# Optimization experiments

Hardware: AMD Instinct MI355X
Metric: run time of the kernel (lower is better)

## Reference

```python
import jax, jax.numpy as jnp
import numpy as np

K = 20
EPS = 1e-5
SLOPE = 0.2


def setup_inputs() -> dict:
    key = jax.random.key(0)
    k1, k2 = jax.random.split(key, 2)
    B, C, N, O = 2, 64, 8192, 64
    x = jax.random.normal(k1, (B, C, N), dtype=jnp.float32)
    W = jax.random.normal(k2, (O, 2 * C), dtype=jnp.float32) * 0.05  # Conv2d 1x1, bias=False
    gamma = jnp.ones((O,), dtype=jnp.float32)
    beta = jnp.zeros((O,), dtype=jnp.float32)
    return {"x": x, "W": W, "gamma": gamma, "beta": beta}


def reference(x, W, gamma, beta):
    # x: (B, C, N)
    B, C, N = x.shape
    xt = jnp.swapaxes(x, 1, 2)  # (B, N, C)

    # --- get_GraphFeatures: KNN by negative squared euclidean distance ---
    inner = jnp.einsum('bnc,bmc->bnm', xt, xt)          # (B, N, N)
    sq = jnp.sum(xt * xt, axis=-1)                      # (B, N)
    neg_dist = 2.0 * inner - sq[:, :, None] - sq[:, None, :]
    _, idx = jax.lax.top_k(neg_dist, K)                 # (B, N, K) int32

    # gather neighbor features: (B, N, K, C)
    nbr = jax.vmap(lambda pts, i: pts[i])(xt, idx)
    center = xt[:, :, None, :]                          # (B, N, 1, C)
    # edge feature: concat(x_j - x_i, x_i) -> (B, N, K, 2C)
    edge = jnp.concatenate([nbr - center, jnp.broadcast_to(center, nbr.shape)], axis=-1)

    # --- 1x1 conv (pointwise GEMM) -> (B, O, N, K) ---
    h = jnp.einsum('bnkf,of->bonk', edge, W)

    # --- BatchNorm2d (training-mode batch stats over B, N, K per channel) ---
    mean = jnp.mean(h, axis=(0, 2, 3), keepdims=True)
    var = jnp.var(h, axis=(0, 2, 3), keepdims=True)
    h = (h - mean) * jax.lax.rsqrt(var + EPS)
    h = h * gamma[None, :, None, None] + beta[None, :, None, None]

    # --- LeakyReLU(0.2) + max over neighbors ---
    h = jnp.where(h >= 0, h, SLOPE * h)
    return jnp.max(h, axis=-1)                          # (B, O, N)
```

## Files before the change

### kernel.cpp

```cpp
#include <hip/hip_runtime.h>
#include <cfloat>

#define BB 2
#define NN 8192
#define OO 64
#define KK 20
#define QB 128
#define MS 16
#define CHUNK 512
#define CAPQ 192
#define RB 8
#define RBS 9

using f16x8  = __attribute__((ext_vector_type(8))) _Float16;
using f32x16 = __attribute__((ext_vector_type(16))) float;
typedef unsigned long long u64;

#define XH_OFF ((size_t)0)
#define XL_OFF (XH_OFF + (size_t)BB*NN*32)
#define SQ_OFF (XL_OFF + (size_t)BB*NN*32)
#define Y1_OFF (SQ_OFF + (size_t)BB*NN)
#define Y2_OFF (Y1_OFF + (size_t)BB*NN*64)
#define TH_OFF (Y2_OFF + (size_t)BB*NN*64)
#define CN_OFF (TH_OFF + (size_t)BB*NN)
#define TL_OFF (CN_OFF + (size_t)BB*NN)
#define CA_OFF (TL_OFF + (size_t)2*BB*NN*KK)
#define IX_OFF (CA_OFF + (size_t)BB*NN*CAPQ*2)
#define HX_OFF (IX_OFF + (size_t)BB*NN*KK)
#define HN_OFF (HX_OFF + (size_t)BB*NN*64)
#define ST_OFF (HN_OFF + (size_t)BB*NN*64)

__device__ __forceinline__ size_t frag_off(int b, int tile, int t, int lane) {
    return ((((size_t)b * (NN / 32) + tile) * 4 + t) * 64 + lane) * 8;
}

__device__ __forceinline__ unsigned fmap(float f) {
    unsigned u = __float_as_uint(f);
    return (u & 0x80000000u) ? ~u : (u | 0x80000000u);
}

__device__ __forceinline__ void sort16(float* v) {
#pragma unroll
    for (int k = 2; k <= 16; k <<= 1) {
#pragma unroll
        for (int j = k >> 1; j > 0; j >>= 1) {
#pragma unroll
            for (int i = 0; i < 16; ++i) {
                int l = i ^ j;
                if (l > i) {
                    bool up = ((i & k) == 0);
                    float mn = fminf(v[i], v[l]);
                    float mx = fmaxf(v[i], v[l]);
                    v[i] = up ? mn : mx;
                    v[l] = up ? mx : mn;
                }
            }
        }
    }
}
__device__ __forceinline__ void bmerge32(float* A) {
#pragma unroll
    for (int j = 16; j > 0; j >>= 1) {
#pragma unroll
        for (int i = 0; i < 32; ++i) {
            if ((i & j) == 0) {
                float mn = fminf(A[i], A[i | j]);
                float mx = fmaxf(A[i], A[i | j]);
                A[i] = mn;
                A[i | j] = mx;
            }
        }
    }
}
__device__ __forceinline__ void merge32_16(float* A, const float* B) {
#pragma unroll
    for (int i = 16; i < 32; ++i) A[i] = fminf(A[i], B[31 - i]);
    bmerge32(A);
}
__device__ __forceinline__ void merge32_32(float* A, const float* B) {
    float t[32];
#pragma unroll
    for (int i = 0; i < 32; ++i) t[i] = fminf(A[i], B[31 - i]);
    bmerge32(t);
#pragma unroll
    for (int i = 0; i < 32; ++i) A[i] = t[i];
}

__device__ __forceinline__ void load_atile(const _Float16* __restrict__ xh,
                                           const _Float16* __restrict__ xl,
                                           int b, int ptile, int lane,
                                           f16x8* Ah, f16x8* Al) {
#pragma unroll
    for (int t = 0; t < 4; ++t) {
        size_t o = frag_off(b, ptile, t, lane);
        Ah[t] = *(const f16x8*)&xh[o];
        Al[t] = *(const f16x8*)&xl[o];
    }
}

__device__ __forceinline__ void dist_from_frags(const f16x8* Ah, const f16x8* Al,
                                                const float* sqs, int sbase, int kh,
                                                const f16x8* Qh, const f16x8* Ql,
                                                float* dv) {
    f32x16 c0, c1;
#pragma unroll
    for (int r2 = 0; r2 < 4; ++r2) {
        float4 sv = *(const float4*)&sqs[sbase + 8 * r2 + 4 * kh];
        c0[4 * r2 + 0] = sv.x;
        c0[4 * r2 + 1] = sv.y;
        c0[4 * r2 + 2] = sv.z;
        c0[4 * r2 + 3] = sv.w;
    }
#pragma unroll
    for (int i = 0; i < 16; ++i) c1[i] = 0.f;
#pragma unroll
    for (int t = 0; t < 4; ++t) {
        c0 = __builtin_amdgcn_mfma_f32_32x32x16_f16(Ah[t], Qh[t], c0, 0, 0, 0);
        c1 = __builtin_amdgcn_mfma_f32_32x32x16_f16(Ah[t], Ql[t], c1, 0, 0, 0);
        c1 = __builtin_amdgcn_mfma_f32_32x32x16_f16(Al[t], Qh[t], c1, 0, 0, 0);
    }
#pragma unroll
    for (int i = 0; i < 16; ++i)
        dv[i] = fmaf(-2.f, c0[i], -9.765625e-4f * c1[i]);
}

__device__ __forceinline__ void load_qfrag(const _Float16* __restrict__ xh,
                                           const _Float16* __restrict__ xl,
                                           int b, int qbase, int lane,
                                           f16x8* Qh, f16x8* Ql) {
    const int qtile = qbase >> 5;
#pragma unroll
    for (int t = 0; t < 4; ++t) {
        size_t o = frag_off(b, qtile, t, lane);
        Qh[t] = *(const f16x8*)&xh[o];
        Ql[t] = *(const f16x8*)&xl[o];
    }
}

__global__ void __launch_bounds__(256, 2)
kA(const float* __restrict__ x, const float* __restrict__ W,
   float* __restrict__ ws) {
    __shared__ __align__(16) float w1s[32 * 64];
    __shared__ __align__(16) float w2s[32 * 64];
    __shared__ float xs[64 * 65];
    __shared__ float tb[64 * 33];
    const int bb = blockIdx.z;
    const int og = blockIdx.y;
    const int obase = og * 32;
    const int nbase = blockIdx.x * 64;
    const int tn = threadIdx.x & 63, tq = threadIdx.x >> 6;

    for (int i = threadIdx.x; i < 2048; i += 256) {
        int ol = i >> 6, c = i & 63;
        float a = W[(obase + ol) * 128 + c];
        float d = W[(obase + ol) * 128 + 64 + c];
        w1s[i] = a;
        w2s[i] = d - a;
    }
    for (int i = threadIdx.x; i < 4096; i += 256) {
        int c = i >> 6, nl = i & 63;
        xs[c * 65 + nl] = x[((size_t)bb * 64 + c) * NN + nbase + nl];
    }
    if (og == 0) {
        if (blockIdx.x == 0 && bb == 0 && threadIdx.x < 128)
            ws[ST_OFF + threadIdx.x] = 0.f;
        int gid = (bb * 128 + blockIdx.x) * 256 + threadIdx.x;
        if (gid < BB * NN) ((int*)(ws + CN_OFF))[gid] = 0;
    }
    __syncthreads();

    float xc[64];
#pragma unroll
    for (int c = 0; c < 64; ++c) xc[c] = xs[c * 65 + tn];

    if (og == 0 && tq == 0) {
        float sqv = 0.f;
#pragma unroll
        for (int c = 0; c < 64; ++c) sqv = fmaf(xc[c], xc[c], sqv);
        int n = nbase + tn;
        ws[SQ_OFF + (size_t)bb * NN + n] = sqv;
        _Float16* xh = (_Float16*)(ws + XH_OFF);
        _Float16* xl = (_Float16*)(ws + XL_OFF);
        int tile = n >> 5, r = n & 31;
#pragma unroll
        for (int t = 0; t < 4; ++t) {
#pragma unroll
            for (int kh = 0; kh < 2; ++kh) {
                f16x8 vh, vl;
#pragma unroll
                for (int j = 0; j < 8; ++j) {
                    float v = xc[t * 16 + kh * 8 + j];
                    _Float16 h = (_Float16)v;
                    vh[j] = h;
                    vl[j] = (_Float16)((v - (float)h) * 2048.f);
                }
                size_t o = frag_off(bb, tile, t, kh * 32 + r);
                *(f16x8*)&xh[o] = vh;
                *(f16x8*)&xl[o] = vl;
            }
        }
    }

    float a1v[8], a2v[8];
#pragma unroll
    for (int o2 = 0; o2 < 8; ++o2) {
        int ol = tq * 8 + o2;
        const float4* w1v = (const float4*)&w1s[ol * 64];
        const float4* w2v = (const float4*)&w2s[ol * 64];
        float a1 = 0.f, a2 = 0.f;
#pragma unroll
        for (int c4 = 0; c4 < 16; ++c4) {
            float4 v1 = w1v[c4];
            float4 v2 = w2v[c4];
            a1 = fmaf(v1.x, xc[4*c4],   a1);
            a1 = fmaf(v1.y, xc[4*c4+1], a1);
            a1 = fmaf(v1.z, xc[4*c4+2], a1);
            a1 = fmaf(v1.w, xc[4*c4+3], a1);
            a2 = fmaf(v2.x, xc[4*c4],   a2);
            a2 = fmaf(v2.y, xc[4*c4+1], a2);
            a2 = fmaf(v2.z, xc[4*c4+2], a2);
            a2 = fmaf(v2.w, xc[4*c4+3], a2);
        }
        a1v[o2] = a1;
        a2v[o2] = a2;
    }

    const int lo = threadIdx.x & 31;
    const int lp = (threadIdx.x >> 5) & 1;
#pragma unroll
    for (int o2 = 0; o2 < 8; ++o2)
        tb[tn * 33 + tq * 8 + o2] = a1v[o2];
    __syncthreads();
#pragma unroll
    for (int j = 0; j < 8; ++j) {
        int r = tq * 16 + 2 * j + lp;
        ws[Y1_OFF + ((size_t)bb * NN + nbase + r) * 64 + obase + lo] = tb[r * 33 + lo];
    }
    __syncthreads();
#pragma unroll
    for (int o2 = 0; o2 < 8; ++o2)
        tb[tn * 33 + tq * 8 + o2] = a2v[o2];
    __syncthreads();
#pragma unroll
    for (int j = 0; j < 8; ++j) {
        int r = tq * 16 + 2 * j + lp;
        ws[Y2_OFF + ((size_t)bb * NN + nbase + r) * 64 + obase + lo] = tb[r * 33 + lo];
    }
}

__global__ void __launch_bounds__(256, 3)
kT(const _Float16* __restrict__ xh, const _Float16* __restrict__ xl,
   const float* __restrict__ sq, float* __restrict__ thrL) {
    __shared__ float mrg[32 * 128];
    __shared__ __align__(16) float sqs[1024];
    const int tid  = threadIdx.x;
    const int lane = tid & 63;
    const int wv   = tid >> 6;
    const int qcol = lane & 31;
    const int kh   = lane >> 5;
    const int b     = blockIdx.y >> 1;
    const int s     = blockIdx.y & 1;
    const int qbase = blockIdx.x * 32;

    for (int i = tid; i < 1024; i += 256)
        sqs[i] = -0.5f * sq[(size_t)b * NN + s * 1024 + i];

    f16x8 Qh[4], Ql[4];
    load_qfrag(xh, xl, b, qbase, lane, Qh, Ql);
    __syncthreads();

    float dk[32];
#pragma unroll
    for (int i = 0; i < 32; ++i) dk[i] = FLT_MAX;

    const int p0 = s * 1024 + wv * 256;
    for (int pt = p0; pt < p0 + 256; pt += 32) {
        f16x8 Ah[4], Al[4];
        load_atile(xh, xl, b, pt >> 5, lane, Ah, Al);
        float dv[16];
        dist_from_frags(Ah, Al, sqs, pt - s * 1024, kh, Qh, Ql, dv);
        float m16 = dv[0];
#pragma unroll
        for (int i = 1; i < 16; ++i) m16 = fminf(m16, dv[i]);
        if (__any(m16 < dk[KK - 1])) {
            sort16(dv);
            merge32_16(dk, dv);
        }
    }

    {
        float B[32];
#pragma unroll
        for (int j = 0; j < 32; ++j) B[j] = __shfl(dk[j], lane | 32);
        merge32_32(dk, B);
    }
    if (kh == 0) {
#pragma unroll
        for (int j = 0; j < 32; ++j) mrg[j * 128 + wv * 32 + qcol] = dk[j];
    }
    __syncthreads();

    if (tid < 32) {
        float B[32];
#pragma unroll 1
        for (int w = 1; w < 4; ++w) {
#pragma unroll
            for (int j = 0; j < 32; ++j) B[j] = mrg[j * 128 + w * 32 + tid];
            merge32_32(dk, B);
        }
        size_t base = (((size_t)b * 2 + s) * NN + qbase + tid) * KK;
#pragma unroll
        for (int j = 0; j < KK; ++j) thrL[base + j] = dk[j];
    }
}

__global__ void kM2(const float* __restrict__ thrL, float* __restrict__ thr) {
    int gid = blockIdx.x * 256 + threadIdx.x;
    int b = gid >> 13, q = gid & (NN - 1);
    float A[KK], Bv[KK];
    const float4* pa = (const float4*)&thrL[(((size_t)b * 2 + 0) * NN + q) * KK];
    const float4* pb = (const float4*)&thrL[(((size_t)b * 2 + 1) * NN + q) * KK];
#pragma unroll
    for (int i = 0; i < 5; ++i) {
        float4 va = pa[i];
        float4 vb = pb[i];
        A[4*i] = va.x;  A[4*i+1] = va.y;  A[4*i+2] = va.z;  A[4*i+3] = va.w;
        Bv[4*i] = vb.x; Bv[4*i+1] = vb.y; Bv[4*i+2] = vb.z; Bv[4*i+3] = vb.w;
    }
    float v = fminf(Bv[KK - 1], A[KK - 1]);
#pragma unroll
    for (int i = 1; i < KK; ++i)
        v = fminf(v, fmaxf(A[i - 1], Bv[KK - 1 - i]));
    thr[gid] = v + fabsf(v) * 1e-6f + 1e-6f;
}

__global__ void __launch_bounds__(256, 4)
kS(const _Float16* __restrict__ xh, const _Float16* __restrict__ xl,
   const float* __restrict__ sq, const float* __restrict__ thr,
   int* __restrict__ cnt, u64* __restrict__ cand) {
    __shared__ u64 lbuf[256 * RBS];
    __shared__ __align__(16) float sqs[CHUNK];
    const int tid  = threadIdx.x;
    const int lane = tid & 63;
    const int wv   = tid >> 6;
    const int qcol = lane & 31;
    const int kh   = lane >> 5;
    const int id     = blockIdx.x;
    const int ychunk = id & 15;
    const int qt     = (id >> 4) & 63;
    const int b      = (id >> 10) & 1;
    const int qbase  = qt * QB + wv * 32;
    const int pbase0 = ychunk * CHUNK;
    const int ptile0 = pbase0 >> 5;

    for (int i = tid; i < CHUNK; i += 256)
        sqs[i] = -0.5f * sq[(size_t)b * NN + pbase0 + i];

    f16x8 Qh[4], Ql[4];
    load_qfrag(xh, xl, b, qbase, lane, Qh, Ql);

    const size_t qidx = (size_t)b * NN + qbase + qcol;
    const float tv = thr[qidx];
    const size_t cb = qidx * CAPQ;
    int c_ = 0;

    __syncthreads();

    auto flushS = [&]() {
        if (c_ > 0) {
            int base = atomicAdd(&cnt[qidx], c_);
#pragma unroll 1
            for (int j = 0; j < c_; ++j) {
                int slot = base + j;
                if (slot < CAPQ) cand[cb + slot] = lbuf[tid * RBS + j];
            }
            c_ = 0;
        }
    };

#pragma unroll 2
    for (int tt = 0; tt < CHUNK / 32; ++tt) {
        f16x8 Ah[4], Al[4];
        load_atile(xh, xl, b, ptile0 + tt, lane, Ah, Al);
        float dv[16];
        dist_from_frags(Ah, Al, sqs, tt * 32, kh, Qh, Ql, dv);

        const int pb4 = pbase0 + tt * 32 + 4 * kh;
#pragma unroll
        for (int i = 0; i < 16; ++i) {
            float d = dv[i];
            if (d <= tv) {
                int id2 = pb4 + ((i & 3) + 8 * (i >> 2));
                lbuf[tid * RBS + c_] = ((u64)fmap(d) << 32) | (unsigned)id2;
                if (++c_ == RB) flushS();
            }
        }
    }
    flushS();
}

__global__ void __launch_bounds__(64)
kP(const int* __restrict__ cnt, const u64* __restrict__ cand,
   int* __restrict__ idxK) {
    const int lane = threadIdx.x;
    const int qloc = lane & 31;
    const int par  = lane >> 5;
    const int q = blockIdx.x * 32 + qloc;
    int m = cnt[q];
    m = m < CAPQ ? m : CAPQ;
    const int nj = (m - par + 1) >> 1;
    u64 kk[KK];
#pragma unroll
    for (int i = 0; i < KK; ++i) kk[i] = ~0ull;

    auto insU = [&](u64 v) {
        kk[KK - 1] = v;
#pragma unroll
        for (int i = KK - 1; i > 0; --i) {
            u64 a = kk[i - 1], c = kk[i];
            bool sw = c < a;
            kk[i - 1] = sw ? c : a;
            kk[i]     = sw ? a : c;
        }
    };

    const u64* cp = &cand[(size_t)q * CAPQ + par];
#pragma unroll 1
    for (int j = 0; j < CAPQ / 2; ++j) {
        if (!__any(j < nj)) break;
        u64 v = cp[2 * j];
        if ((j < nj) && v < kk[KK - 1]) insU(v);
    }

#pragma unroll
    for (int j = 0; j < KK; ++j) {
        u64 v = __shfl(kk[j], lane | 32);
        bool ins = (par == 0) && v < kk[KK - 1];
        if (!__any(ins)) break;
        if (ins) insU(v);
    }

    if (par == 0) {
        int* op = &idxK[(size_t)q * KK];
#pragma unroll
        for (int i = 0; i < KK; ++i) op[i] = (int)(unsigned)(kk[i] & 0xffffffffu);
    }
}

__global__ void kC1(const float* __restrict__ y1, const float* __restrict__ y2,
                    const int* __restrict__ idxK, float* __restrict__ hmaxT,
                    float* __restrict__ hminT, float* __restrict__ stats) {
    __shared__ int li[32 * KK];
    __shared__ float red[256];
    __shared__ float thm[32 * 65];
    __shared__ float thn[32 * 65];
    int b = blockIdx.y;
    int o = threadIdx.x & 63;
    int nn = threadIdx.x >> 6;
    int nbase = blockIdx.x * 32;

    for (int i = threadIdx.x; i < 32 * KK; i += 256)
        li[i] = idxK[((size_t)b * NN + nbase) * KK + i];
    __syncthreads();

    float s = 0.f, ss = 0.f;
    for (int gidx = 0; gidx < 8; ++gidx) {
        int nl = gidx * 4 + nn;
        int n = nbase + nl;
        float y2v = y2[((size_t)b * NN + n) * 64 + o];
        float hm = -FLT_MAX, hn = FLT_MAX;
        const int* lin = &li[nl * KK];
#pragma unroll 4
        for (int k = 0; k < KK; ++k) {
            int j = lin[k];
            float h = y1[((size_t)b * NN + j) * 64 + o] + y2v;
            s += h;
            ss += h * h;
            hm = fmaxf(hm, h);
            hn = fminf(hn, h);
        }
        thm[nl * 65 + o] = hm;
        thn[nl * 65 + o] = hn;
    }
    __syncthreads();

    int l = threadIdx.x & 31, g = threadIdx.x >> 5;
#pragma unroll
    for (int i = 0; i < 8; ++i) {
        int o2 = g * 8 + i;
        hmaxT[((size_t)b * 64 + o2) * NN + nbase + l] = thm[l * 65 + o2];
        hminT[((size_t)b * 64 + o2) * NN + nbase + l] = thn[l * 65 + o2];
    }

    __syncthreads();
    red[threadIdx.x] = s;
    __syncthreads();
    if (threadIdx.x < 64) {
        float v = red[o] + red[64 + o] + red[128 + o] + red[192 + o];
        atomicAdd(&stats[o], v);
    }
    __syncthreads();
    red[threadIdx.x] = ss;
    __syncthreads();
    if (threadIdx.x < 64) {
        float v = red[o] + red[64 + o] + red[128 + o] + red[192 + o];
        atomicAdd(&stats[64 + o], v);
    }
}

__global__ void kC3(const float* __restrict__ hmaxT, const float* __restrict__ hminT,
                    const float* __restrict__ stats, const float* __restrict__ gamma,
                    const float* __restrict__ beta, float* __restrict__ out) {
    int o = blockIdx.x;
    int half = blockIdx.y;
    int b = blockIdx.z;
    const float c = (float)BB * NN * KK;
    float mean = stats[o] / c;
    float var = stats[64 + o] / c - mean * mean;
    float rs = rsqrtf(var + 1e-5f);
    float a = gamma[o] * rs;
    float b2 = beta[o] - a * mean;
    size_t rowb = ((size_t)b * 64 + o) * NN;
    int n0 = half * (NN / 2), n1 = n0 + NN / 2;
    for (int n = n0 + threadIdx.x; n < n1; n += 256) {
        float hm = hmaxT[rowb + n];
        float hn = hminT[rowb + n];
        float hs = (a >= 0.f) ? hm : hn;
        float v = a * hs + b2;
        v = (v >= 0.f) ? v : 0.2f * v;
        out[rowb + n] = v;
    }
}

extern "C" void kernel_launch(void* const* d_in, const int* in_sizes, int n_in,
                              void* d_out, int out_size, void* d_ws, size_t ws_size,
                              hipStream_t stream) {
    const float* x     = (const float*)d_in[0];
    const float* W     = (const float*)d_in[1];
    const float* gamma = (const float*)d_in[2];
    const float* beta  = (const float*)d_in[3];
    float* out = (float*)d_out;
    float* ws  = (float*)d_ws;

    _Float16* xh = (_Float16*)(ws + XH_OFF);
    _Float16* xl = (_Float16*)(ws + XL_OFF);
    float* sq    = ws + SQ_OFF;
    float* y1    = ws + Y1_OFF;
    float* y2    = ws + Y2_OFF;
    float* thr   = ws + TH_OFF;
    int*   cnt   = (int*)(ws + CN_OFF);
    float* thrL  = ws + TL_OFF;
    u64*   cand  = (u64*)(ws + CA_OFF);
    int*   idxK  = (int*)(ws + IX_OFF);
    float* hmaxT = ws + HX_OFF;
    float* hminT = ws + HN_OFF;
    float* stats = ws + ST_OFF;

    kA<<<dim3(NN / 64, 2, BB), 256, 0, stream>>>(x, W, ws);
    kT<<<dim3(NN / 32, 2 * BB), 256, 0, stream>>>(xh, xl, sq, thrL);
    kM2<<<dim3(BB * NN / 256), 256, 0, stream>>>(thrL, thr);
    kS<<<dim3(MS * (NN / QB) * BB), 256, 0, stream>>>(xh, xl, sq, thr, cnt, cand);
    kP<<<dim3(BB * NN / 32), 64, 0, stream>>>(cnt, cand, idxK);
    kC1<<<dim3(NN / 32, BB), 256, 0, stream>>>(y1, y2, idxK, hmaxT, hminT, stats);
    kC3<<<dim3(OO, 2, BB), 256, 0, stream>>>(hmaxT, hminT, stats, gamma, beta, out);
}
```

Before: 261.2 us.

## Replace per-thread insertion top-k with wave-wide rank counting selection

The candidate selection kernel used to assign each query to two threads, each running a serial 20-element insertion sort over up to 192 candidates, then merged them through shuffles. Now a whole 64-lane wave handles one query: each lane holds up to three candidates, computes each one's rank by broadcasting every candidate with shuffles and counting smaller keys, and scatters the candidates with rank below K directly to the output. This removes the long serial compare-swap chains and the divergent inserts in exchange for O(m) shuffles per lane and 8x more waves. It relies on the packed distance/index keys being unique so the ranks do not collide.

```diff
diff --git a/kernel.cpp b/kernel.cpp
--- a/kernel.cpp
+++ b/kernel.cpp
@@ -399,52 +399,50 @@
     flushS();
 }
 
-__global__ void __launch_bounds__(64)
+__global__ void __launch_bounds__(256, 4)
 kP(const int* __restrict__ cnt, const u64* __restrict__ cand,
    int* __restrict__ idxK) {
-    const int lane = threadIdx.x;
-    const int qloc = lane & 31;
-    const int par  = lane >> 5;
-    const int q = blockIdx.x * 32 + qloc;
+    const int lane = threadIdx.x & 63;
+    const int wq   = threadIdx.x >> 6;
+    const int q    = blockIdx.x * 4 + wq;
     int m = cnt[q];
     m = m < CAPQ ? m : CAPQ;
-    const int nj = (m - par + 1) >> 1;
-    u64 kk[KK];
-#pragma unroll
-    for (int i = 0; i < KK; ++i) kk[i] = ~0ull;
-
-    auto insU = [&](u64 v) {
-        kk[KK - 1] = v;
-#pragma unroll
-        for (int i = KK - 1; i > 0; --i) {
-            u64 a = kk[i - 1], c = kk[i];
-            bool sw = c < a;
-            kk[i - 1] = sw ? c : a;
-            kk[i]     = sw ? a : c;
-        }
-    };
-
-    const u64* cp = &cand[(size_t)q * CAPQ + par];
-#pragma unroll 1
-    for (int j = 0; j < CAPQ / 2; ++j) {
-        if (!__any(j < nj)) break;
-        u64 v = cp[2 * j];
-        if ((j < nj) && v < kk[KK - 1]) insU(v);
-    }
-
-#pragma unroll
-    for (int j = 0; j < KK; ++j) {
-        u64 v = __shfl(kk[j], lane | 32);
-        bool ins = (par == 0) && v < kk[KK - 1];
-        if (!__any(ins)) break;
-        if (ins) insU(v);
-    }
-
-    if (par == 0) {
-        int* op = &idxK[(size_t)q * KK];
-#pragma unroll
-        for (int i = 0; i < KK; ++i) op[i] = (int)(unsigned)(kk[i] & 0xffffffffu);
-    }
+    const u64* cp = &cand[(size_t)q * CAPQ];
+
+    u64 v0 = (lane       < m) ? cp[lane]       : ~0ull;
+    u64 v1 = (lane + 64  < m) ? cp[lane + 64]  : ~0ull;
+    u64 v2 = (lane + 128 < m) ? cp[lane + 128] : ~0ull;
+    int r0 = 0, r1 = 0, r2 = 0;
+
+    {
+        const int cap0 = m < 64 ? m : 64;
+#pragma unroll 4
+        for (int jj = 0; jj < cap0; ++jj) {
+            u64 bv = __shfl(v0, jj);
+            r0 += (bv < v0); r1 += (bv < v1); r2 += (bv < v2);
+        }
+    }
+    if (m > 64) {
+        const int cap1 = (m - 64) < 64 ? (m - 64) : 64;
+#pragma unroll 4
+        for (int jj = 0; jj < cap1; ++jj) {
+            u64 bv = __shfl(v1, jj);
+            r0 += (bv < v0); r1 += (bv < v1); r2 += (bv < v2);
+        }
+    }
+    if (m > 128) {
+        const int cap2 = (m - 128) < 64 ? (m - 128) : 64;
+#pragma unroll 4
+        for (int jj = 0; jj < cap2; ++jj) {
+            u64 bv = __shfl(v2, jj);
+            r0 += (bv < v0); r1 += (bv < v1); r2 += (bv < v2);
+        }
+    }
+
+    int* op = &idxK[(size_t)q * KK];
+    if (lane       < m && r0 < KK) op[r0] = (int)(unsigned)(v0 & 0xffffffffu);
+    if (lane + 64  < m && r1 < KK) op[r1] = (int)(unsigned)(v1 & 0xffffffffu);
+    if (lane + 128 < m && r2 < KK) op[r2] = (int)(unsigned)(v2 & 0xffffffffu);
 }
 
 __global__ void kC1(const float* __restrict__ y1, const float* __restrict__ y2,
@@ -560,7 +558,7 @@
     kT<<<dim3(NN / 32, 2 * BB), 256, 0, stream>>>(xh, xl, sq, thrL);
     kM2<<<dim3(BB * NN / 256), 256, 0, stream>>>(thrL, thr);
     kS<<<dim3(MS * (NN / QB) * BB), 256, 0, stream>>>(xh, xl, sq, thr, cnt, cand);
-    kP<<<dim3(BB * NN / 32), 64, 0, stream>>>(cnt, cand, idxK);
+    kP<<<dim3(BB * NN / 4), 256, 0, stream>>>(cnt, cand, idxK);
     kC1<<<dim3(NN / 32, BB), 256, 0, stream>>>(y1, y2, idxK, hmaxT, hminT, stats);
     kC3<<<dim3(OO, 2, BB), 256, 0, stream>>>(hmaxT, hminT, stats, gamma, beta, out);
 }
```

New measurement: 250.7 us, median of 3. 1.04x faster.
